# Optimization experiments

Hardware: AMD Instinct MI355X
Metric: run time of the kernel (lower is better)

The kernel has to match this reference:

```python
import jax, jax.numpy as jnp
import numpy as np


def setup_inputs() -> dict:
    key = jax.random.key(0)
    kA, kB = jax.random.split(key)
    B, H, W, C = 1, 80, 80, 256  # NHWC backbone features; B must be 1 for the TF broadcast in the divide to be valid
    feature_A = jax.random.normal(kA, (B, H, W, C), dtype=jnp.float32)
    feature_B = jax.random.normal(kB, (B, H, W, C), dtype=jnp.float32)
    return {"feature_A": feature_A, "feature_B": feature_B}


def reference(feature_A, feature_B):
    # corr[b,i,j,k,l] = mean_c A[b,i,j,c] * B[b,k,l,c]
    # Expressed as a batched matmul instead of materializing the (H,W,H,W,C) intermediate.
    C = feature_A.shape[-1]
    corr = jnp.einsum('bijc,bklc->bijkl', feature_A, feature_B) / C  # [B,H,W,H,W]
    # penalty[b,i,j] = sqrt(sum_{k,l} corr^2)
    penalty = jnp.sqrt(jnp.sum(corr * corr, axis=(-1, -2)))  # [B,H,W]
    # Faithful to tf.math.divide: trailing-dim broadcasting of [B,H,W] against [B,H,W,H,W]
    # (valid because B == 1; penalty aligns to the (j,k,l) trailing axes exactly as in TF).
    return corr / penalty
```

## Files before the change

### kernel.cpp

```cpp
#include <hip/hip_runtime.h>

typedef __attribute__((ext_vector_type(8))) short bf16x8;
typedef __attribute__((ext_vector_type(4))) float f32x4;

#define M_TOT 6400
#define C_TOT 256
#define BM 128
#define BN 128
#define BK 32
#define NTILE 50

#define VMCNT0 asm volatile("s_waitcnt vmcnt(0)" ::: "memory")
#define VMCNT4 asm volatile("s_waitcnt vmcnt(4)" ::: "memory")
#define SBAR   __builtin_amdgcn_s_barrier()

__device__ __forceinline__ short f2bf(float f) {
    unsigned u = __float_as_uint(f);
    u = (u + 0x7fffu + ((u >> 16) & 1u)) >> 16;
    return (short)u;
}
__device__ __forceinline__ float bf2f(short s) {
    return __uint_as_float(((unsigned)(unsigned short)s) << 16);
}

__device__ __forceinline__ void gload16(const short* g, short* l) {
    __builtin_amdgcn_global_load_lds(
        (const __attribute__((address_space(1))) void*)g,
        (__attribute__((address_space(3))) void*)l, 16, 0, 0);
}


__global__ __launch_bounds__(256) void prep(const float* __restrict__ A,
                                            const float* __restrict__ Bm,
                                            short* __restrict__ Ab,
                                            short* __restrict__ Bb,
                                            short* __restrict__ Bt,
                                            float* __restrict__ P)
{
    __shared__ __align__(16) short Lb[64][72];
    const int bid = blockIdx.x;
    const int t   = threadIdx.x;

    if (bid < 400) {
        const int n0 = (bid % 100) * 64;
        const int c0 = (bid / 100) * 64;
        const int r  = t >> 2;
        const int cb = (t & 3) * 16;

        const float4* src = reinterpret_cast<const float4*>(
            Bm + (size_t)(n0 + r) * C_TOT + c0 + cb);
        const float4 v0 = src[0], v1 = src[1], v2 = src[2], v3 = src[3];
        bf16x8 w0, w1;
        w0[0]=f2bf(v0.x); w0[1]=f2bf(v0.y); w0[2]=f2bf(v0.z); w0[3]=f2bf(v0.w);
        w0[4]=f2bf(v1.x); w0[5]=f2bf(v1.y); w0[6]=f2bf(v1.z); w0[7]=f2bf(v1.w);
        w1[0]=f2bf(v2.x); w1[1]=f2bf(v2.y); w1[2]=f2bf(v2.z); w1[3]=f2bf(v2.w);
        w1[4]=f2bf(v3.x); w1[5]=f2bf(v3.y); w1[6]=f2bf(v3.z); w1[7]=f2bf(v3.w);
        *reinterpret_cast<bf16x8*>(&Lb[r][cb])     = w0;
        *reinterpret_cast<bf16x8*>(&Lb[r][cb + 8]) = w1;
        short* brow = Bb + (size_t)(n0 + r) * C_TOT + c0 + cb;
        *reinterpret_cast<bf16x8*>(brow)     = w0;
        *reinterpret_cast<bf16x8*>(brow + 8) = w1;
        __syncthreads();

        #pragma unroll
        for (int p = 0; p < 2; ++p) {
            const int q = t + p * 256;
            const int c = q >> 3;
            const int h = q & 7;
            bf16x8 w;
            #pragma unroll
            for (int j = 0; j < 8; ++j) w[j] = Lb[h * 8 + j][c];
            *reinterpret_cast<bf16x8*>(&Bt[(size_t)(c0 + c) * M_TOT + n0 + h * 8]) = w;
        }
    } else {
        const int aid = bid - 400;
        if (aid == 0)
            for (int j = t; j < M_TOT; j += 256) P[j] = 0.0f;
        const int base = aid * 2048;
        #pragma unroll
        for (int it = 0; it < 8; ++it) {
            const int i = base + it * 256 + t;
            const float4 v0 = reinterpret_cast<const float4*>(A + (size_t)i * 8)[0];
            const float4 v1 = reinterpret_cast<const float4*>(A + (size_t)i * 8)[1];
            bf16x8 w;
            w[0]=f2bf(v0.x); w[1]=f2bf(v0.y); w[2]=f2bf(v0.z); w[3]=f2bf(v0.w);
            w[4]=f2bf(v1.x); w[5]=f2bf(v1.y); w[6]=f2bf(v1.z); w[7]=f2bf(v1.w);
            *reinterpret_cast<bf16x8*>(Ab + (size_t)i * 8) = w;
        }
    }
}

__global__ __launch_bounds__(256) void convert_ab(const float* __restrict__ A,
                                                  const float* __restrict__ Bm,
                                                  short* __restrict__ Ab,
                                                  short* __restrict__ Bb)
{
    const int n8 = M_TOT * C_TOT / 8;
    for (int i = blockIdx.x * blockDim.x + threadIdx.x; i < 2 * n8;
         i += gridDim.x * blockDim.x) {
        const float* s = (i < n8) ? (A + (size_t)i * 8) : (Bm + (size_t)(i - n8) * 8);
        short* d       = (i < n8) ? (Ab + (size_t)i * 8) : (Bb + (size_t)(i - n8) * 8);
        const float4 v0 = reinterpret_cast<const float4*>(s)[0];
        const float4 v1 = reinterpret_cast<const float4*>(s)[1];
        bf16x8 w;
        w[0]=f2bf(v0.x); w[1]=f2bf(v0.y); w[2]=f2bf(v0.z); w[3]=f2bf(v0.w);
        w[4]=f2bf(v1.x); w[5]=f2bf(v1.y); w[6]=f2bf(v1.z); w[7]=f2bf(v1.w);
        *reinterpret_cast<bf16x8*>(d) = w;
    }
}


__device__ __forceinline__ void stage_tiles_g(const short* __restrict__ A,
                                              const short* __restrict__ B,
                                              int m0, int n0, int k0,
                                              int lda, int ldb,
                                              short* As, short* Bs,
                                              int wave, int lane)
{
    #pragma unroll
    for (int t = 0; t < 2; ++t) {
        const int c  = (wave * 2 + t) * 64 + lane;
        const int r  = c >> 2;
        const int g  = c & 3;
        const int sg = g ^ ((r >> 1) & 3);
        gload16(A + (size_t)(m0 + r) * lda + k0 + sg * 8, As + (wave * 2 + t) * 512);
        gload16(B + (size_t)(n0 + r) * ldb + k0 + sg * 8, Bs + (wave * 2 + t) * 512);
    }
}

template<int KSTEPS>
__device__ __forceinline__ void gemm_tile_g(const short* __restrict__ A,
                                            const short* __restrict__ B,
                                            int m0, int n0, int kbase,
                                            int lda, int ldb, int tid,
                                            short (*Sm)[2][4096],
                                            f32x4 acc[4][4])
{
    const int lane = tid & 63;
    const int wave = tid >> 6;
    const int rl   = lane & 15;
    const int g_rd = lane >> 4;
    const int wr   = wave >> 1;
    const int wc   = wave & 1;

    stage_tiles_g(A, B, m0, n0, kbase, lda, ldb, &Sm[0][0][0], &Sm[0][1][0], wave, lane);
    if (KSTEPS > 1)
        stage_tiles_g(A, B, m0, n0, kbase + BK, lda, ldb,
                      &Sm[1][0][0], &Sm[1][1][0], wave, lane);
    if (KSTEPS > 1) { VMCNT4; } else { VMCNT0; }
    SBAR;

    #pragma unroll
    for (int kt = 0; kt < KSTEPS; ++kt) {
        const int cur = kt % 3;
        if (kt + 2 < KSTEPS)
            stage_tiles_g(A, B, m0, n0, kbase + (kt + 2) * BK, lda, ldb,
                          &Sm[(kt + 2) % 3][0][0], &Sm[(kt + 2) % 3][1][0], wave, lane);

        bf16x8 af[4], bfr[4];
        #pragma unroll
        for (int mi = 0; mi < 4; ++mi) {
            const int r  = wr * 64 + mi * 16 + rl;
            const int sg = g_rd ^ ((r >> 1) & 3);
            af[mi] = *reinterpret_cast<const bf16x8*>(&Sm[cur][0][r * BK + sg * 8]);
        }
        #pragma unroll
        for (int ni = 0; ni < 4; ++ni) {
            const int r  = wc * 64 + ni * 16 + rl;
            const int sg = g_rd ^ ((r >> 1) & 3);
            bfr[ni] = *reinterpret_cast<const bf16x8*>(&Sm[cur][1][r * BK + sg * 8]);
        }
        __builtin_amdgcn_s_setprio(1);
        #pragma unroll
        for (int mi = 0; mi < 4; ++mi)
            #pragma unroll
            for (int ni = 0; ni < 4; ++ni)
                acc[mi][ni] = __builtin_amdgcn_mfma_f32_16x16x32_bf16(
                    af[mi], bfr[ni], acc[mi][ni], 0, 0, 0);
        __builtin_amdgcn_s_setprio(0);

        if (kt + 1 < KSTEPS) {
            if (kt + 2 < KSTEPS) { VMCNT4; } else { VMCNT0; }
            SBAR;
        }
    }
}


template<int STEPS>
__global__ __launch_bounds__(256) void gemm_G(const short* __restrict__ Bt,
                                              float* __restrict__ Gp)
{
    __shared__ __align__(16) short Sm[3][2][4096];
    const int tid = threadIdx.x;
    const int m0 = blockIdx.y * BM, n0 = blockIdx.x * BN;
    const int z  = blockIdx.z;
    f32x4 acc[4][4] = {};
    gemm_tile_g<STEPS>(Bt, Bt, m0, n0, z * (STEPS * BK),
                       M_TOT, M_TOT, tid, Sm, acc);

    float* dst = Gp + (size_t)z * (C_TOT * C_TOT);
    const int lane = tid & 63, rl = lane & 15;
    const int wave = tid >> 6, wr = wave >> 1, wc = wave & 1;
    #pragma unroll
    for (int mi = 0; mi < 4; ++mi)
        #pragma unroll
        for (int i = 0; i < 4; ++i) {
            const int m = m0 + wr * 64 + mi * 16 + (lane >> 4) * 4 + i;
            #pragma unroll
            for (int ni = 0; ni < 4; ++ni)
                dst[m * C_TOT + n0 + wc * 64 + ni * 16 + rl] = acc[mi][ni][i];
        }
}

__global__ __launch_bounds__(256) void g_reduce(const float* __restrict__ Gp,
                                                short* __restrict__ Gb,
                                                int nchunks)
{
    const int i4 = blockIdx.x * 256 + threadIdx.x;
    float4 s = make_float4(0.f, 0.f, 0.f, 0.f);
    for (int z = 0; z < nchunks; ++z) {
        const float4 v = reinterpret_cast<const float4*>(
            Gp + (size_t)z * (C_TOT * C_TOT))[i4];
        s.x += v.x; s.y += v.y; s.z += v.z; s.w += v.w;
    }
    short4 o;
    o.x = f2bf(s.x); o.y = f2bf(s.y); o.z = f2bf(s.z); o.w = f2bf(s.w);
    reinterpret_cast<short4*>(Gb)[i4] = o;
}

__global__ __launch_bounds__(256) void penalty_q(const short* __restrict__ Ab,
                                                 const short* __restrict__ Gb,
                                                 float* __restrict__ P)
{
    __shared__ __align__(16) short Sm[3][2][4096];
    const int tid = threadIdx.x;
    const int m0 = blockIdx.x * BM;
    const int ci = blockIdx.y & 1, cj = blockIdx.y >> 1;
    const int lane = tid & 63, rl = lane & 15;
    const int wave = tid >> 6, wr = wave >> 1, wc = wave & 1;

    f32x4 acc[4][4] = {};
    gemm_tile_g<4>(Ab, Gb + (size_t)(cj * BM) * C_TOT, m0, 0, ci * BM,
                   C_TOT, C_TOT, tid, Sm, acc);

    #pragma unroll
    for (int mi = 0; mi < 4; ++mi)
        #pragma unroll
        for (int i = 0; i < 4; ++i) {
            const int m = m0 + wr * 64 + mi * 16 + (lane >> 4) * 4 + i;
            float s = 0.0f;
            #pragma unroll
            for (int ni = 0; ni < 4; ++ni) {
                const int cp = cj * BM + wc * 64 + ni * 16 + rl;
                s += acc[mi][ni][i] * bf2f(Ab[(size_t)m * C_TOT + cp]);
            }
            s += __shfl_xor(s, 1);
            s += __shfl_xor(s, 2);
            s += __shfl_xor(s, 4);
            s += __shfl_xor(s, 8);
            if (rl == 0) atomicAdd(&P[m], s);
        }
}


__global__ __launch_bounds__(256) void gemm_out(const short* __restrict__ Ab,
                                                const short* __restrict__ Bb,
                                                const float* __restrict__ P,
                                                float* __restrict__ out)
{
    __shared__ __align__(16) short Sm[3][2][4096];
    const int tid = threadIdx.x;
    const int lane = tid & 63, rl = lane & 15;
    const int wave = tid >> 6, wr = wave >> 1, wc = wave & 1;

    const int nwg = NTILE * NTILE, q = nwg >> 3, r = nwg & 7;
    const int orig = blockIdx.x;
    const int xcd = orig & 7, idx = orig >> 3;
    const int wg = (xcd < r ? xcd * (q + 1) : r * (q + 1) + (xcd - r) * q) + idx;
    const int m0 = (wg / NTILE) * BM;
    const int n0 = (wg % NTILE) * BN;

    f32x4 acc[4][4] = {};
    gemm_tile_g<8>(Ab, Bb, m0, n0, 0, C_TOT, C_TOT, tid, Sm, acc);

    float rs[4];
    #pragma unroll
    for (int ni = 0; ni < 4; ++ni)
        rs[ni] = rsqrtf(P[n0 + wc * 64 + ni * 16 + rl]);

    SBAR;

    float* Es = reinterpret_cast<float*>(Sm) + wave * 1088;
    #pragma unroll
    for (int mi = 0; mi < 4; ++mi) {
        #pragma unroll
        for (int ni = 0; ni < 4; ++ni)
            #pragma unroll
            for (int i = 0; i < 4; ++i)
                Es[((lane >> 4) * 4 + i) * 68 + ni * 16 + rl] = acc[mi][ni][i] * rs[ni];
        #pragma unroll
        for (int it = 0; it < 4; ++it) {
            const int f   = it * 64 + lane;
            const int row = f >> 4;
            const int c4  = f & 15;
            const float4 v = *reinterpret_cast<const float4*>(&Es[row * 68 + c4 * 4]);
            const int m = m0 + wr * 64 + mi * 16 + row;
            *reinterpret_cast<float4*>(&out[(size_t)m * M_TOT + n0 + wc * 64 + c4 * 4]) = v;
        }
    }
}


__global__ __launch_bounds__(256) void gemm_penalty(const short* __restrict__ Ab,
                                                    const short* __restrict__ Bb,
                                                    float* __restrict__ P)
{
    __shared__ __align__(16) short Sm[3][2][4096];
    const int tid = threadIdx.x;
    const int m0 = blockIdx.y * BM, n0 = blockIdx.x * BN;
    f32x4 acc[4][4] = {};
    gemm_tile_g<8>(Ab, Bb, m0, n0, 0, C_TOT, C_TOT, tid, Sm, acc);

    const int lane = tid & 63, rl = lane & 15;
    const int wave = tid >> 6, wr = wave >> 1;
    #pragma unroll
    for (int mi = 0; mi < 4; ++mi) {
        #pragma unroll
        for (int i = 0; i < 4; ++i) {
            const int m = m0 + wr * 64 + mi * 16 + (lane >> 4) * 4 + i;
            float s = 0.0f;
            #pragma unroll
            for (int ni = 0; ni < 4; ++ni) {
                const float v = acc[mi][ni][i];
                s += v * v;
            }
            s += __shfl_xor(s, 1);
            s += __shfl_xor(s, 2);
            s += __shfl_xor(s, 4);
            s += __shfl_xor(s, 8);
            if (rl == 0) atomicAdd(&P[m], s);
        }
    }
}

__global__ __launch_bounds__(256) void gemm_out_plain(const short* __restrict__ Ab,
                                                      const short* __restrict__ Bb,
                                                      const float* __restrict__ P,
                                                      float* __restrict__ out)
{
    __shared__ __align__(16) short Sm[3][2][4096];
    const int tid = threadIdx.x;
    const int lane = tid & 63, rl = lane & 15;
    const int wave = tid >> 6, wr = wave >> 1, wc = wave & 1;
    const int m0 = blockIdx.y * BM, n0 = blockIdx.x * BN;

    f32x4 acc[4][4] = {};
    gemm_tile_g<8>(Ab, Bb, m0, n0, 0, C_TOT, C_TOT, tid, Sm, acc);

    float rs[4];
    #pragma unroll
    for (int ni = 0; ni < 4; ++ni)
        rs[ni] = rsqrtf(P[n0 + wc * 64 + ni * 16 + rl]);

    SBAR;

    float* Es = reinterpret_cast<float*>(Sm) + wave * 1088;
    #pragma unroll
    for (int mi = 0; mi < 4; ++mi) {
        #pragma unroll
        for (int ni = 0; ni < 4; ++ni)
            #pragma unroll
            for (int i = 0; i < 4; ++i)
                Es[((lane >> 4) * 4 + i) * 68 + ni * 16 + rl] = acc[mi][ni][i] * rs[ni];
        #pragma unroll
        for (int it = 0; it < 4; ++it) {
            const int f   = it * 64 + lane;
            const int row = f >> 4;
            const int c4  = f & 15;
            const float4 v = *reinterpret_cast<const float4*>(&Es[row * 68 + c4 * 4]);
            const int m = m0 + wr * 64 + mi * 16 + row;
            *reinterpret_cast<float4*>(&out[(size_t)m * M_TOT + n0 + wc * 64 + c4 * 4]) = v;
        }
    }
}


__global__ __launch_bounds__(256) void corr_gemm(const float* __restrict__ A,
                                                 const float* __restrict__ Bm,
                                                 float* __restrict__ out,
                                                 float* __restrict__ penalty)
{
    __shared__ short As[BM * BK];
    __shared__ short Bs[BN * BK];

    const int tid  = threadIdx.x;
    const int lane = tid & 63;
    const int wave = tid >> 6;
    const int wr   = wave >> 1;
    const int wc   = wave & 1;
    const int m0   = blockIdx.y * BM;
    const int n0   = blockIdx.x * BN;
    const int g_rd = lane >> 4;
    const int rl   = lane & 15;

    f32x4 acc[4][4] = {};

    for (int k0 = 0; k0 < C_TOT; k0 += BK) {
        #pragma unroll
        for (int half = 0; half < 2; ++half) {
            const int cc = tid + half * 256;
            const int r  = cc >> 2;
            const int g  = cc & 3;
            const int sg = g ^ ((r >> 1) & 3);

            const float4* pa = reinterpret_cast<const float4*>(
                A + (size_t)(m0 + r) * C_TOT + k0 + g * 8);
            float4 a0 = pa[0], a1 = pa[1];
            bf16x8 wa;
            wa[0]=f2bf(a0.x); wa[1]=f2bf(a0.y); wa[2]=f2bf(a0.z); wa[3]=f2bf(a0.w);
            wa[4]=f2bf(a1.x); wa[5]=f2bf(a1.y); wa[6]=f2bf(a1.z); wa[7]=f2bf(a1.w);
            *reinterpret_cast<bf16x8*>(&As[r * BK + sg * 8]) = wa;

            const float4* pb = reinterpret_cast<const float4*>(
                Bm + (size_t)(n0 + r) * C_TOT + k0 + g * 8);
            float4 b0 = pb[0], b1 = pb[1];
            bf16x8 wb;
            wb[0]=f2bf(b0.x); wb[1]=f2bf(b0.y); wb[2]=f2bf(b0.z); wb[3]=f2bf(b0.w);
            wb[4]=f2bf(b1.x); wb[5]=f2bf(b1.y); wb[6]=f2bf(b1.z); wb[7]=f2bf(b1.w);
            *reinterpret_cast<bf16x8*>(&Bs[r * BK + sg * 8]) = wb;
        }
        __syncthreads();

        bf16x8 af[4], bfr[4];
        #pragma unroll
        for (int mi = 0; mi < 4; ++mi) {
            const int r  = wr * 64 + mi * 16 + rl;
            const int sg = g_rd ^ ((r >> 1) & 3);
            af[mi] = *reinterpret_cast<const bf16x8*>(&As[r * BK + sg * 8]);
        }
        #pragma unroll
        for (int ni = 0; ni < 4; ++ni) {
            const int r  = wc * 64 + ni * 16 + rl;
            const int sg = g_rd ^ ((r >> 1) & 3);
            bfr[ni] = *reinterpret_cast<const bf16x8*>(&Bs[r * BK + sg * 8]);
        }
        #pragma unroll
        for (int mi = 0; mi < 4; ++mi)
            #pragma unroll
            for (int ni = 0; ni < 4; ++ni)
                acc[mi][ni] = __builtin_amdgcn_mfma_f32_16x16x32_bf16(
                    af[mi], bfr[ni], acc[mi][ni], 0, 0, 0);
        __syncthreads();
    }

    const float inv_c = 1.0f / (float)C_TOT;
    #pragma unroll
    for (int mi = 0; mi < 4; ++mi) {
        #pragma unroll
        for (int i = 0; i < 4; ++i) {
            const int m = m0 + wr * 64 + mi * 16 + (lane >> 4) * 4 + i;
            float s = 0.0f;
            #pragma unroll
            for (int ni = 0; ni < 4; ++ni) {
                const float v = acc[mi][ni][i] * inv_c;
                out[(size_t)m * M_TOT + n0 + wc * 64 + ni * 16 + rl] = v;
                s += v * v;
            }
            s += __shfl_xor(s, 1);
            s += __shfl_xor(s, 2);
            s += __shfl_xor(s, 4);
            s += __shfl_xor(s, 8);
            if (rl == 0) atomicAdd(&penalty[m], s);
        }
    }
}

__global__ __launch_bounds__(256) void scale_k(float* __restrict__ out,
                                               const float* __restrict__ penalty)
{
    const unsigned cols4 = M_TOT / 4;
    const unsigned total = (unsigned)M_TOT * cols4;
    float4* o4 = reinterpret_cast<float4*>(out);
    const float4* p4 = reinterpret_cast<const float4*>(penalty);
    for (unsigned idx = blockIdx.x * blockDim.x + threadIdx.x; idx < total;
         idx += gridDim.x * blockDim.x) {
        const unsigned n4 = idx % cols4;
        const float4 p = p4[n4];
        float4 v = o4[idx];
        v.x *= rsqrtf(p.x);
        v.y *= rsqrtf(p.y);
        v.z *= rsqrtf(p.z);
        v.w *= rsqrtf(p.w);
        o4[idx] = v;
    }
}


extern "C" void kernel_launch(void* const* d_in, const int* in_sizes, int n_in,
                              void* d_out, int out_size, void* d_ws, size_t ws_size,
                              hipStream_t stream) {
    const float* A = (const float*)d_in[0];
    const float* B = (const float*)d_in[1];
    float* out     = (float*)d_out;

    const size_t mat_sh = (size_t)M_TOT * C_TOT;
    const size_t sz_ab  = mat_sh * sizeof(short);
    const size_t sz_gb  = (size_t)C_TOT * C_TOT * sizeof(short);
    const size_t sz_p   = (size_t)M_TOT * sizeof(float);
    const size_t sz_gq  = (size_t)C_TOT * C_TOT * sizeof(float);
    const size_t base_need = 3 * sz_ab + sz_gb + sz_p;
    const size_t need_f40  = base_need + 40 * sz_gq;
    const size_t need_f20  = base_need + 20 * sz_gq;
    const size_t need_mid  = 2 * sz_ab + sz_p;

    dim3 grid2(NTILE, NTILE);

    if (ws_size >= need_f20) {
        short* Ab = (short*)d_ws;
        short* Bb = Ab + mat_sh;
        short* Bt = Bb + mat_sh;
        short* Gb = Bt + mat_sh;
        float* P  = (float*)((char*)d_ws + 3 * sz_ab + sz_gb);
        float* Gp = (float*)((char*)d_ws + 3 * sz_ab + sz_gb + sz_p);

        prep<<<500, 256, 0, stream>>>(A, B, Ab, Bb, Bt, P);
        if (ws_size >= need_f40) {
            gemm_G<5><<<dim3(2, 2, 40), 256, 0, stream>>>(Bt, Gp);
            g_reduce<<<64, 256, 0, stream>>>(Gp, Gb, 40);
        } else {
            gemm_G<10><<<dim3(2, 2, 20), 256, 0, stream>>>(Bt, Gp);
            g_reduce<<<64, 256, 0, stream>>>(Gp, Gb, 20);
        }
        penalty_q<<<dim3(NTILE, 4), 256, 0, stream>>>(Ab, Gb, P);
        gemm_out<<<NTILE * NTILE, 256, 0, stream>>>(Ab, Bb, P, out);
    } else if (ws_size >= need_mid) {
        short* Ab = (short*)d_ws;
        short* Bb = Ab + mat_sh;
        float* P  = (float*)(Bb + mat_sh);

        hipMemsetAsync(P, 0, sz_p, stream);
        convert_ab<<<1600, 256, 0, stream>>>(A, B, Ab, Bb);
        gemm_penalty<<<grid2, dim3(256), 0, stream>>>(Ab, Bb, P);
        gemm_out_plain<<<grid2, dim3(256), 0, stream>>>(Ab, Bb, P, out);
    } else {
        float* penalty = (float*)d_ws;
        hipMemsetAsync(penalty, 0, sz_p, stream);
        corr_gemm<<<grid2, dim3(256), 0, stream>>>(A, B, out, penalty);
        scale_k<<<2048, 256, 0, stream>>>(out, penalty);
    }
}
```

Measured before the change: 85.01 us.

## Widen output GEMM tile to 128x256 with custom triple-buffered staging

The output GEMM now computes 128x256 tiles per workgroup instead of 128x128, halving the grid and reusing each A tile across twice as many columns. It adds an inlined triple-buffered k-loop with XOR-swizzled LDS staging, MFMA priority raising and launch bounds requesting two blocks per CU. The epilogue is widened to stage 8 column fragments through LDS before float4 stores. This raises register pressure (32 accumulators per lane) and cuts the number of workgroups, which may hurt occupancy or tail balance on a store-bound kernel.

```diff
diff --git a/kernel.cpp b/kernel.cpp
--- a/kernel.cpp
+++ b/kernel.cpp
@@ -9,9 +9,12 @@
 #define BN 128
 #define BK 32
 #define NTILE 50
+#define ONM 50
+#define ONN 25
 
 #define VMCNT0 asm volatile("s_waitcnt vmcnt(0)" ::: "memory")
 #define VMCNT4 asm volatile("s_waitcnt vmcnt(4)" ::: "memory")
+#define VMCNT6 asm volatile("s_waitcnt vmcnt(6)" ::: "memory")
 #define SBAR   __builtin_amdgcn_s_barrier()
 
 __device__ __forceinline__ short f2bf(float f) {
@@ -264,49 +267,115 @@
 }
 
 
-__global__ __launch_bounds__(256) void gemm_out(const short* __restrict__ Ab,
-                                                const short* __restrict__ Bb,
-                                                const float* __restrict__ P,
-                                                float* __restrict__ out)
-{
-    __shared__ __align__(16) short Sm[3][2][4096];
+#define OBUF 12288
+#define OB_B 4096
+
+__device__ __forceinline__ void stage_tiles_o(const short* __restrict__ A,
+                                              const short* __restrict__ B,
+                                              int m0, int n0, int k0,
+                                              short* buf, int wave, int lane)
+{
+    #pragma unroll
+    for (int t = 0; t < 2; ++t) {
+        const int c  = (wave * 2 + t) * 64 + lane;
+        const int r  = c >> 2;
+        const int g  = c & 3;
+        const int sg = g ^ ((r >> 1) & 3);
+        gload16(A + (size_t)(m0 + r) * C_TOT + k0 + sg * 8, buf + (wave * 2 + t) * 512);
+    }
+    #pragma unroll
+    for (int t = 0; t < 4; ++t) {
+        const int c  = (wave * 4 + t) * 64 + lane;
+        const int r  = c >> 2;
+        const int g  = c & 3;
+        const int sg = g ^ ((r >> 1) & 3);
+        gload16(B + (size_t)(n0 + r) * C_TOT + k0 + sg * 8,
+                buf + OB_B + (wave * 4 + t) * 512);
+    }
+}
+
+__global__ __launch_bounds__(256, 2) void gemm_out(const short* __restrict__ Ab,
+                                                   const short* __restrict__ Bb,
+                                                   const float* __restrict__ P,
+                                                   float* __restrict__ out)
+{
+    __shared__ __align__(16) short Sm[3][OBUF];
     const int tid = threadIdx.x;
     const int lane = tid & 63, rl = lane & 15;
+    const int g_rd = lane >> 4;
     const int wave = tid >> 6, wr = wave >> 1, wc = wave & 1;
 
-    const int nwg = NTILE * NTILE, q = nwg >> 3, r = nwg & 7;
+    const int nwg = ONM * ONN, q = nwg >> 3, r = nwg & 7;
     const int orig = blockIdx.x;
     const int xcd = orig & 7, idx = orig >> 3;
     const int wg = (xcd < r ? xcd * (q + 1) : r * (q + 1) + (xcd - r) * q) + idx;
-    const int m0 = (wg / NTILE) * BM;
-    const int n0 = (wg % NTILE) * BN;
-
-    f32x4 acc[4][4] = {};
-    gemm_tile_g<8>(Ab, Bb, m0, n0, 0, C_TOT, C_TOT, tid, Sm, acc);
-
-    float rs[4];
-    #pragma unroll
-    for (int ni = 0; ni < 4; ++ni)
-        rs[ni] = rsqrtf(P[n0 + wc * 64 + ni * 16 + rl]);
+    const int m0 = (wg / ONN) * 128;
+    const int n0 = (wg % ONN) * 256;
+
+    f32x4 acc[4][8] = {};
+
+    stage_tiles_o(Ab, Bb, m0, n0, 0,  &Sm[0][0], wave, lane);
+    stage_tiles_o(Ab, Bb, m0, n0, BK, &Sm[1][0], wave, lane);
+    VMCNT6; SBAR;
+
+    #pragma unroll
+    for (int kt = 0; kt < 8; ++kt) {
+        const int cur = kt % 3;
+        if (kt + 2 < 8)
+            stage_tiles_o(Ab, Bb, m0, n0, (kt + 2) * BK, &Sm[(kt + 2) % 3][0], wave, lane);
+
+        bf16x8 af[4], bfr[8];
+        #pragma unroll
+        for (int mi = 0; mi < 4; ++mi) {
+            const int rr = wr * 64 + mi * 16 + rl;
+            const int sg = g_rd ^ ((rr >> 1) & 3);
+            af[mi] = *reinterpret_cast<const bf16x8*>(&Sm[cur][rr * BK + sg * 8]);
+        }
+        #pragma unroll
+        for (int ni = 0; ni < 8; ++ni) {
+            const int rr = wc * 128 + ni * 16 + rl;
+            const int sg = g_rd ^ ((rr >> 1) & 3);
+            bfr[ni] = *reinterpret_cast<const bf16x8*>(&Sm[cur][OB_B + rr * BK + sg * 8]);
+        }
+        __builtin_amdgcn_s_setprio(1);
+        #pragma unroll
+        for (int mi = 0; mi < 4; ++mi)
+            #pragma unroll
+            for (int ni = 0; ni < 8; ++ni)
+                acc[mi][ni] = __builtin_amdgcn_mfma_f32_16x16x32_bf16(
+                    af[mi], bfr[ni], acc[mi][ni], 0, 0, 0);
+        __builtin_amdgcn_s_setprio(0);
+
+        if (kt + 1 < 8) {
+            if (kt + 2 < 8) { VMCNT6; } else { VMCNT0; }
+            SBAR;
+        }
+    }
+
+    float rs[8];
+    #pragma unroll
+    for (int ni = 0; ni < 8; ++ni)
+        rs[ni] = rsqrtf(P[n0 + wc * 128 + ni * 16 + rl]);
 
     SBAR;
 
-    float* Es = reinterpret_cast<float*>(Sm) + wave * 1088;
+    float* Es = reinterpret_cast<float*>(Sm) + wave * 2112;
     #pragma unroll
     for (int mi = 0; mi < 4; ++mi) {
         #pragma unroll
-        for (int ni = 0; ni < 4; ++ni)
+        for (int ni = 0; ni < 8; ++ni)
             #pragma unroll
             for (int i = 0; i < 4; ++i)
-                Es[((lane >> 4) * 4 + i) * 68 + ni * 16 + rl] = acc[mi][ni][i] * rs[ni];
-        #pragma unroll
-        for (int it = 0; it < 4; ++it) {
+                Es[((lane >> 4) * 4 + i) * 132 + ni * 16 + rl] = acc[mi][ni][i] * rs[ni];
+        #pragma unroll
+        for (int it = 0; it < 8; ++it) {
             const int f   = it * 64 + lane;
-            const int row = f >> 4;
-            const int c4  = f & 15;
-            const float4 v = *reinterpret_cast<const float4*>(&Es[row * 68 + c4 * 4]);
+            const int row = f >> 5;
+            const int c4  = f & 31;
+            const float4 v = *reinterpret_cast<const float4*>(&Es[row * 132 + c4 * 4]);
             const int m = m0 + wr * 64 + mi * 16 + row;
-            *reinterpret_cast<float4*>(&out[(size_t)m * M_TOT + n0 + wc * 64 + c4 * 4]) = v;
+            *reinterpret_cast<float4*>(
+                &out[(size_t)m * M_TOT + n0 + wc * 128 + c4 * 4]) = v;
         }
     }
 }
@@ -533,7 +602,7 @@
             g_reduce<<<64, 256, 0, stream>>>(Gp, Gb, 20);
         }
         penalty_q<<<dim3(NTILE, 4), 256, 0, stream>>>(Ab, Gb, P);
-        gemm_out<<<NTILE * NTILE, 256, 0, stream>>>(Ab, Bb, P, out);
+        gemm_out<<<ONM * ONN, 256, 0, stream>>>(Ab, Bb, P, out);
     } else if (ws_size >= need_mid) {
         short* Ab = (short*)d_ws;
         short* Bb = Ab + mat_sh;
```

Result: no change. 84.01 us (-1.2%).
